# Performance work log

Hardware: AMD Instinct MI355X
Metric: run time of the kernel (lower is better)

## Reference

```python
import jax, jax.numpy as jnp
import numpy as np
from jax import lax

MAX_DIST_THR = 10.0
R = 10  # window radius: any distance < thr has per-axis offset <= 9, so R=10 is exact after clamping
INF = jnp.float32(1e12)


def _min_pass(c, axis):
    # 1D min-convolution with squared offsets: out[i] = min_k (c[i+k-R] + (k-R)^2)
    n = c.shape[axis]
    pad = [(0, 0)] * c.ndim
    pad[axis] = (R, R)
    p = jnp.pad(c, pad, constant_values=INF)
    out = None
    for k in range(2 * R + 1):
        v = lax.slice_in_dim(p, k, k + n, axis=axis) + jnp.float32((k - R) ** 2)
        out = v if out is None else jnp.minimum(out, v)
    return out


def _clamped_edt(fg):
    # Euclidean distance to nearest True pixel, exact where < MAX_DIST_THR, clamped above.
    cost = jnp.where(fg, jnp.float32(0.0), INF)  # [B,1,H,W]
    d2 = _min_pass(_min_pass(cost, 2), 3)
    return jnp.minimum(jnp.sqrt(d2), jnp.float32(MAX_DIST_THR))


def reference(gt, pred):
    thr = jnp.float32(MAX_DIST_THR)
    D_gt = lax.stop_gradient(_clamped_edt(gt > 0.5))
    D_est = lax.stop_gradient(_clamped_edt(pred > 0.5))
    mask_D_gt = D_gt < thr
    filt_sum = jnp.sum(pred * mask_D_gt)
    # ch[ch > thr] = thr  ==  minimum (values are non-negative)
    ch1 = jnp.minimum(D_gt * pred, thr)
    ch2 = jnp.minimum(D_est * gt, thr)
    num = jnp.sum(ch1 + ch2, axis=(1, 2, 3))  # [B]
    den = jnp.mean(jnp.sum(pred, axis=(1, 2, 3)) + jnp.sum(gt, axis=(1, 2, 3)))  # scalar
    dbe_com = num / den
    return jnp.where(filt_sum == 0, thr, dbe_com)


def setup_inputs() -> dict:
    key = jax.random.key(0)
    k1, k2 = jax.random.split(key)
    shape = (1, 1, 2048, 4096)
    gt = jax.random.bernoulli(k1, 0.05, shape).astype(jnp.float32)
    pred = jax.random.bernoulli(k2, 0.05, shape).astype(jnp.float32)
    return {"gt": gt, "pred": pred}
```

## Files before the change

### kernel.cpp

```cpp
#include <hip/hip_runtime.h>

typedef unsigned long long u64;
typedef unsigned int u32;

#define HH 2048
#define WW 4096
#define MW 66
#define MROWS (HH + 20)
#define MASK_WORDS ((size_t)MROWS * MW)
#define MASK_BYTES (MASK_WORDS * 8)
#define THR 10.0f
#define LIST_CAP (512u * 1024u)

#define PACK_BLOCKS 2048
#define COMP_BLOCKS 256
#define SCAN_BLOCKS 1024

#define GM_OFF 16384
#define PM_OFF (GM_OFF + MASK_BYTES)
#define LP_OFF (PM_OFF + MASK_BYTES)
#define LG_OFF (LP_OFF + LIST_CAP * 4)

__global__ __launch_bounds__(256) void pack_masks(const float* __restrict__ gt,
                                                  const float* __restrict__ pred,
                                                  u64* __restrict__ gm,
                                                  u64* __restrict__ pm) {
    int l = threadIdx.x & 63;
    int gw = (blockIdx.x * 256 + threadIdx.x) >> 6;
    #pragma unroll 1
    for (int t = 0; t < 4; ++t) {
        int tile = gw * 4 + t;
        int base = tile * 256;
        u64 g0 = __ballot(gt[base +   0 + l] > 0.5f);
        u64 g1 = __ballot(gt[base +  64 + l] > 0.5f);
        u64 g2 = __ballot(gt[base + 128 + l] > 0.5f);
        u64 g3 = __ballot(gt[base + 192 + l] > 0.5f);
        u64 p0 = __ballot(pred[base +   0 + l] > 0.5f);
        u64 p1 = __ballot(pred[base +  64 + l] > 0.5f);
        u64 p2 = __ballot(pred[base + 192 - 64 + l] > 0.5f);
        u64 p3 = __ballot(pred[base + 192 + l] > 0.5f);
        if (l < 4) {
            u64 gv = (l == 0) ? g0 : (l == 1) ? g1 : (l == 2) ? g2 : g3;
            u64 pv = (l == 0) ? p0 : (l == 1) ? p1 : (l == 2) ? p2 : p3;
            int W = tile * 4 + l;
            size_t o = (size_t)((W >> 6) + 10) * MW + 1 + (W & 63);
            gm[o] = gv;
            pm[o] = pv;
        }
    }
}

__global__ __launch_bounds__(256) void compact(const u64* __restrict__ gm,
                                               const u64* __restrict__ pm,
                                               u32* __restrict__ cnt,
                                               u32* __restrict__ listP,
                                               u32* __restrict__ listG) {
    bool isPred = blockIdx.x < (COMP_BLOCKS / 2);
    const u64* msk = isPred ? pm : gm;
    u32* lst = isPred ? listP : listG;
    u32* ctr = isPred ? cnt : cnt + 1;
    int wb = (blockIdx.x & (COMP_BLOCKS / 2 - 1)) * 1024;
    int tid = threadIdx.x;

    u64 wv[4];
    u32 pc[4];
    u32 tp = 0;
    #pragma unroll
    for (int j = 0; j < 4; ++j) {
        int W = wb + tid + 256 * j;
        wv[j] = msk[(size_t)((W >> 6) + 10) * MW + 1 + (W & 63)];
        pc[j] = (u32)__popcll(wv[j]);
        tp += pc[j];
    }
    u32 s = tp;
    #pragma unroll
    for (int o = 1; o < 64; o <<= 1) {
        u32 v = __shfl_up(s, o);
        if ((tid & 63) >= o) s += v;
    }
    u32 excl = s - tp;
    __shared__ u32 wtot[4], wbase[4], sbase;
    int wid = tid >> 6, lane = tid & 63;
    if (lane == 63) wtot[wid] = s;
    __syncthreads();
    if (tid == 0) {
        u32 bt = 0;
        for (int i = 0; i < 4; ++i) { wbase[i] = bt; bt += wtot[i]; }
        sbase = atomicAdd(ctr, bt);
    }
    __syncthreads();
    u32 ptr = sbase + wbase[wid] + excl;
    #pragma unroll
    for (int j = 0; j < 4; ++j) {
        int W = wb + tid + 256 * j;
        u32 yx = ((u32)(W >> 6) << 12) | ((u32)(W & 63) << 6);
        u64 m = wv[j];
        while (m) {
            u32 b = (u32)__ffsll((long long)m) - 1u;
            if (ptr < LIST_CAP) lst[ptr] = yx + b;
            ++ptr;
            m &= m - 1;
        }
    }
}

__device__ __forceinline__ u32 scan_d2(const u64* __restrict__ rowc, int x) {
    int b = x + 54;
    int sh = b & 63;
    int shl = 63 - sh;
    const u64* q = rowc + (b >> 6);
    u64 q0 = q[0], q1 = q[1];
    u32 win = (u32)((q0 >> sh) | ((q1 << 1) << shl)) & 0x1FFFFFu;
    u32 hi = win >> 10;
    u32 lo = win & 0x3FFu;
    u32 dr = (u32)__ffs((int)hi) - 1u;
    u32 dl = (u32)__clz((int)lo) - 21u;
    u32 mdx = dr < dl ? dr : dl;
    u32 mind2 = mdx * mdx;
    #pragma unroll
    for (int ady = 1; ady <= 9; ++ady) {
        const u64* r0 = q - (size_t)ady * MW;
        const u64* r1 = q + (size_t)ady * MW;
        u64 a0 = r0[0] | r1[0];
        u64 a1 = r0[1] | r1[1];
        u32 w = (u32)((a0 >> sh) | ((a1 << 1) << shl)) & 0x1FFFFFu;
        u32 h2 = w >> 10;
        u32 l2 = w & 0x3FFu;
        u32 d1 = (u32)__ffs((int)h2) - 1u;
        u32 d0 = (u32)__clz((int)l2) - 21u;
        u32 m2 = d1 < d0 ? d1 : d0;
        u32 d2 = (u32)(ady * ady) + m2 * m2;
        mind2 = d2 < mind2 ? d2 : mind2;
    }
    return mind2;
}

__global__ __launch_bounds__(256) void dbe_scan(const u64* __restrict__ gm,
                                                const u64* __restrict__ pm,
                                                const u32* __restrict__ cnt,
                                                const u32* __restrict__ listP,
                                                const u32* __restrict__ listG,
                                                float* __restrict__ pn,
                                                float* __restrict__ pf) {
    u32 cp = cnt[0], cg = cnt[1];
    u32 total = cp + cg;
    float num = 0.0f, filt = 0.0f;

    for (u32 i = blockIdx.x * 256 + threadIdx.x; i < total;
         i += SCAN_BLOCKS * 256) {
        bool isP = i < cp;
        const u32* ep = isP ? (listP + i) : (listG + (i - cp));
        u32 e = *ep;
        u32 x = e & 4095u;
        u32 y = e >> 12;
        const u64* base = isP ? gm : pm;
        u32 d2 = scan_d2(base + (size_t)(y + 10) * MW, (int)x);
        num += fminf(sqrtf((float)d2), THR);
        filt += (isP && d2 < 100u) ? 1.0f : 0.0f;
    }

    #pragma unroll
    for (int o = 32; o > 0; o >>= 1) {
        num += __shfl_down(num, o);
        filt += __shfl_down(filt, o);
    }
    __shared__ float sN[4], sF[4];
    int lane = threadIdx.x & 63, wid = threadIdx.x >> 6;
    if (lane == 0) { sN[wid] = num; sF[wid] = filt; }
    __syncthreads();
    if (threadIdx.x == 0) {
        pn[blockIdx.x] = sN[0] + sN[1] + sN[2] + sN[3];
        pf[blockIdx.x] = sF[0] + sF[1] + sF[2] + sF[3];
    }
}

__global__ __launch_bounds__(256) void dbe_reduce(const float* __restrict__ pn,
                                                  const float* __restrict__ pf,
                                                  const u32* __restrict__ cnt,
                                                  float* __restrict__ out) {
    double n = 0.0, f = 0.0;
    for (int i = threadIdx.x; i < SCAN_BLOCKS; i += 256) {
        n += (double)pn[i];
        f += (double)pf[i];
    }
    #pragma unroll
    for (int o = 32; o > 0; o >>= 1) {
        n += __shfl_down(n, o);
        f += __shfl_down(f, o);
    }
    __shared__ double sn[4], sf[4];
    int lane = threadIdx.x & 63, wid = threadIdx.x >> 6;
    if (lane == 0) { sn[wid] = n; sf[wid] = f; }
    __syncthreads();
    if (threadIdx.x == 0) {
        double N = sn[0] + sn[1] + sn[2] + sn[3];
        double F = sf[0] + sf[1] + sf[2] + sf[3];
        double den = (double)(cnt[0] + cnt[1]);
        out[0] = (F == 0.0) ? THR : (float)(N / den);
    }
}

extern "C" void kernel_launch(void* const* d_in, const int* in_sizes, int n_in,
                              void* d_out, int out_size, void* d_ws, size_t ws_size,
                              hipStream_t stream) {
    const float* gt   = (const float*)d_in[0];
    const float* pred = (const float*)d_in[1];
    float* out = (float*)d_out;

    char* ws = (char*)d_ws;
    u32* cnt = (u32*)ws;
    float* pn = (float*)(ws + 256);
    float* pf = (float*)(ws + 4352);
    u64* gm = (u64*)(ws + GM_OFF);
    u64* pm = (u64*)(ws + PM_OFF);
    u32* listP = (u32*)(ws + LP_OFF);
    u32* listG = (u32*)(ws + LG_OFF);

    hipMemsetAsync(d_ws, 0, LP_OFF, stream);

    pack_masks<<<PACK_BLOCKS, 256, 0, stream>>>(gt, pred, gm, pm);
    compact<<<COMP_BLOCKS, 256, 0, stream>>>(gm, pm, cnt, listP, listG);
    dbe_scan<<<SCAN_BLOCKS, 256, 0, stream>>>(gm, pm, cnt, listP, listG, pn, pf);
    dbe_reduce<<<1, 256, 0, stream>>>(pn, pf, cnt, out);
}
```

Measured before the change: 116.9 us.

## Replace workspace memset with in-kernel guard zeroing and fuse final reduce

Removes the large hipMemsetAsync over both bit-mask buffers and instead has pack_masks zero only the counters and the padding border words (top/bottom 10 rows and left/right edge words). The separate single-block reduce kernel is folded into dbe_scan using a last-block ticket counter with threadfences. This cuts a multi-megabyte memset and one kernel launch, at the cost of relying on correct guard-region coverage and an atomic ticket. It also fixes the pred p2 index typo (same offset, cosmetic).

```diff
diff --git a/kernel.cpp b/kernel.cpp
--- a/kernel.cpp
+++ b/kernel.cpp
@@ -15,6 +15,7 @@
 #define PACK_BLOCKS 2048
 #define COMP_BLOCKS 256
 #define SCAN_BLOCKS 1024
+#define GUARD_WORDS 5416
 
 #define GM_OFF 16384
 #define PM_OFF (GM_OFF + MASK_BYTES)
@@ -24,9 +25,25 @@
 __global__ __launch_bounds__(256) void pack_masks(const float* __restrict__ gt,
                                                   const float* __restrict__ pred,
                                                   u64* __restrict__ gm,
-                                                  u64* __restrict__ pm) {
+                                                  u64* __restrict__ pm,
+                                                  u32* __restrict__ cnt) {
+    int gtid = blockIdx.x * 256 + threadIdx.x;
+    if (gtid < 3) cnt[gtid] = 0u;
+    if (gtid < 2 * GUARD_WORDS) {
+        int m = gtid >= GUARD_WORDS;
+        int i = gtid - m * GUARD_WORDS;
+        u64* dst = m ? pm : gm;
+        int row, w;
+        if (i < 660)       { row = i / 66;            w = i - row * 66; }
+        else if (i < 1320) { int j = i - 660; int r = j / 66;
+                             row = (MROWS - 10) + r;  w = j - r * 66; }
+        else               { int j = i - 1320; row = 10 + (j >> 1);
+                             w = (j & 1) ? (MW - 1) : 0; }
+        dst[(size_t)row * MW + w] = 0ull;
+    }
+
     int l = threadIdx.x & 63;
-    int gw = (blockIdx.x * 256 + threadIdx.x) >> 6;
+    int gw = gtid >> 6;
     #pragma unroll 1
     for (int t = 0; t < 4; ++t) {
         int tile = gw * 4 + t;
@@ -37,7 +54,7 @@
         u64 g3 = __ballot(gt[base + 192 + l] > 0.5f);
         u64 p0 = __ballot(pred[base +   0 + l] > 0.5f);
         u64 p1 = __ballot(pred[base +  64 + l] > 0.5f);
-        u64 p2 = __ballot(pred[base + 192 - 64 + l] > 0.5f);
+        u64 p2 = __ballot(pred[base + 128 + l] > 0.5f);
         u64 p3 = __ballot(pred[base + 192 + l] > 0.5f);
         if (l < 4) {
             u64 gv = (l == 0) ? g0 : (l == 1) ? g1 : (l == 2) ? g2 : g3;
@@ -63,14 +80,12 @@
     int tid = threadIdx.x;
 
     u64 wv[4];
-    u32 pc[4];
     u32 tp = 0;
     #pragma unroll
     for (int j = 0; j < 4; ++j) {
         int W = wb + tid + 256 * j;
         wv[j] = msk[(size_t)((W >> 6) + 10) * MW + 1 + (W & 63)];
-        pc[j] = (u32)__popcll(wv[j]);
-        tp += pc[j];
+        tp += (u32)__popcll(wv[j]);
     }
     u32 s = tp;
     #pragma unroll
@@ -137,11 +152,12 @@
 
 __global__ __launch_bounds__(256) void dbe_scan(const u64* __restrict__ gm,
                                                 const u64* __restrict__ pm,
-                                                const u32* __restrict__ cnt,
+                                                u32* __restrict__ cnt,
                                                 const u32* __restrict__ listP,
                                                 const u32* __restrict__ listG,
                                                 float* __restrict__ pn,
-                                                float* __restrict__ pf) {
+                                                float* __restrict__ pf,
+                                                float* __restrict__ out) {
     u32 cp = cnt[0], cg = cnt[1];
     u32 total = cp + cg;
     float num = 0.0f, filt = 0.0f;
@@ -149,8 +165,7 @@
     for (u32 i = blockIdx.x * 256 + threadIdx.x; i < total;
          i += SCAN_BLOCKS * 256) {
         bool isP = i < cp;
-        const u32* ep = isP ? (listP + i) : (listG + (i - cp));
-        u32 e = *ep;
+        u32 e = isP ? listP[i] : listG[i - cp];
         u32 x = e & 4095u;
         u32 y = e >> 12;
         const u64* base = isP ? gm : pm;
@@ -165,19 +180,20 @@
         filt += __shfl_down(filt, o);
     }
     __shared__ float sN[4], sF[4];
+    __shared__ u32 ticket;
     int lane = threadIdx.x & 63, wid = threadIdx.x >> 6;
     if (lane == 0) { sN[wid] = num; sF[wid] = filt; }
     __syncthreads();
     if (threadIdx.x == 0) {
         pn[blockIdx.x] = sN[0] + sN[1] + sN[2] + sN[3];
         pf[blockIdx.x] = sF[0] + sF[1] + sF[2] + sF[3];
-    }
-}
-
-__global__ __launch_bounds__(256) void dbe_reduce(const float* __restrict__ pn,
-                                                  const float* __restrict__ pf,
-                                                  const u32* __restrict__ cnt,
-                                                  float* __restrict__ out) {
+        __threadfence();
+        ticket = atomicAdd(&cnt[2], 1u);
+    }
+    __syncthreads();
+    if (ticket != SCAN_BLOCKS - 1) return;
+
+    __threadfence();
     double n = 0.0, f = 0.0;
     for (int i = threadIdx.x; i < SCAN_BLOCKS; i += 256) {
         n += (double)pn[i];
@@ -189,13 +205,12 @@
         f += __shfl_down(f, o);
     }
     __shared__ double sn[4], sf[4];
-    int lane = threadIdx.x & 63, wid = threadIdx.x >> 6;
     if (lane == 0) { sn[wid] = n; sf[wid] = f; }
     __syncthreads();
     if (threadIdx.x == 0) {
         double N = sn[0] + sn[1] + sn[2] + sn[3];
         double F = sf[0] + sf[1] + sf[2] + sf[3];
-        double den = (double)(cnt[0] + cnt[1]);
+        double den = (double)total;
         out[0] = (F == 0.0) ? THR : (float)(N / den);
     }
 }
@@ -216,10 +231,8 @@
     u32* listP = (u32*)(ws + LP_OFF);
     u32* listG = (u32*)(ws + LG_OFF);
 
-    hipMemsetAsync(d_ws, 0, LP_OFF, stream);
-
-    pack_masks<<<PACK_BLOCKS, 256, 0, stream>>>(gt, pred, gm, pm);
+    pack_masks<<<PACK_BLOCKS, 256, 0, stream>>>(gt, pred, gm, pm, cnt);
     compact<<<COMP_BLOCKS, 256, 0, stream>>>(gm, pm, cnt, listP, listG);
-    dbe_scan<<<SCAN_BLOCKS, 256, 0, stream>>>(gm, pm, cnt, listP, listG, pn, pf);
-    dbe_reduce<<<1, 256, 0, stream>>>(pn, pf, cnt, out);
-}
+    dbe_scan<<<SCAN_BLOCKS, 256, 0, stream>>>(gm, pm, cnt, listP, listG,
+                                              pn, pf, out);
+}
```

Result: slower. 133.6 us (+14.3%).
